# Performance work log

Measured on AMD Instinct MI355X. Metric: run time of the kernel, lower is better.

## Reference

```python
import jax, jax.numpy as jnp
import numpy as np

DIM = 1024
NUM_HEAD = 16
DIM_HEAD = DIM // NUM_HEAD
MAX_SEQ_LEN = 4096
RMS_EPS = 1.1920928955078125e-07  # torch nn.RMSNorm default eps = finfo(fp32).eps
LIN_EPS = 1e-6
PAD_VAL = 1.0
THETA = 10000.0


def rmsnorm(x, g):
    return x * jax.lax.rsqrt(jnp.mean(x * x, axis=-1, keepdims=True) + RMS_EPS) * g


def setup_inputs() -> dict:
    key = jax.random.key(0)
    ks = jax.random.split(key, 20)
    B, L, C, D = 4, 2048, 256, DIM
    s = 1.0 / np.sqrt(D)
    inp = {
        "x": jax.random.normal(ks[0], (B, L, D), jnp.float32),
        "context": jax.random.normal(ks[1], (B, C, D), jnp.float32),
        "attn_mask": jax.random.randint(ks[2], (B, L, L), 0, 2).astype(bool),
        "start_pos": jax.random.randint(ks[3], (B,), 0, MAX_SEQ_LEN - L).astype(jnp.int64),
        "Wqkv": jax.random.normal(ks[4], (D, 3 * D), jnp.float32) * s,
        "bqkv": jax.random.normal(ks[5], (3 * D,), jnp.float32) * 0.01,
        "g_q": jnp.ones((D,), jnp.float32),
        "g_k": jnp.ones((D,), jnp.float32),
        "cWqkv": jax.random.normal(ks[6], (D, 3 * D), jnp.float32) * s,
        "cbqkv": jax.random.normal(ks[7], (3 * D,), jnp.float32) * 0.01,
        "cg_q": jnp.ones((D,), jnp.float32),
        "cg_k": jnp.ones((D,), jnp.float32),
        "Wout": jax.random.normal(ks[8], (D, D), jnp.float32) * s,
        "bout": jax.random.normal(ks[9], (D,), jnp.float32) * 0.01,
        "g_out": jnp.ones((D,), jnp.float32),
        "cWout": jax.random.normal(ks[10], (D, D), jnp.float32) * s,
        "cbout": jax.random.normal(ks[11], (D,), jnp.float32) * 0.01,
        "cg_out": jnp.ones((D,), jnp.float32),
    }
    return inp


def _freqs(pos_indices):
    # pos_indices: (B, L) int
    inv = 1.0 / (THETA ** (jnp.arange(0, DIM_HEAD, 2, dtype=jnp.float32) / DIM_HEAD))  # (DH/2,)
    ang = pos_indices.astype(jnp.float32)[..., None] * inv  # (B, L, DH/2)
    return jnp.cos(ang), jnp.sin(ang)


def _apply_rope(t, cos, sin):
    # t: (B, H, L, DH); cos/sin: (B, L, DH/2) -> broadcast over head
    B, H, L, DH = t.shape
    tr = t.reshape(B, H, L, DH // 2, 2)
    t0, t1 = tr[..., 0], tr[..., 1]
    c = cos[:, None]  # (B,1,L,DH/2)
    s = sin[:, None]
    out = jnp.stack([t0 * c - t1 * s, t0 * s + t1 * c], axis=-1)
    return out.reshape(B, H, L, DH)


def _split_heads(t):
    B, L, D = t.shape
    return t.reshape(B, L, NUM_HEAD, DIM_HEAD).transpose(0, 2, 1, 3)


def _augment_mask(m, C):
    # m: (B, L, L) bool -> (B, L+C, L+C) bool
    B, L, _ = m.shape
    c_to_seq = jnp.broadcast_to(jnp.any(m, axis=1, keepdims=True), (B, C, L))
    seq_to_c = jnp.broadcast_to(jnp.any(m, axis=2, keepdims=True), (B, L, C))
    c_to_c = jnp.ones((B, C, C), bool)
    top = jnp.concatenate([m, seq_to_c], axis=2)
    bot = jnp.concatenate([c_to_seq, c_to_c], axis=2)
    return jnp.concatenate([top, bot], axis=1)


def reference(x, context, attn_mask, start_pos, Wqkv, bqkv, g_q, g_k,
              cWqkv, cbqkv, cg_q, cg_k, Wout, bout, g_out, cWout, cbout, cg_out):
    B, L, D = x.shape
    C = context.shape[1]

    q, k, v = jnp.split(x @ Wqkv + bqkv, 3, axis=-1)
    q = rmsnorm(q, g_q)
    k = rmsnorm(k, g_k)
    q, k, v = _split_heads(q), _split_heads(k), _split_heads(v)  # (B,H,L,DH)

    pos = start_pos[:, None] + jnp.arange(L, dtype=start_pos.dtype)[None]  # (B,L)
    cos, sin = _freqs(pos)
    q = _apply_rope(q, cos, sin)
    k = _apply_rope(k, cos, sin)

    cq, ck, cv = jnp.split(context @ cWqkv + cbqkv, 3, axis=-1)
    cq = rmsnorm(cq, cg_q)
    ck = rmsnorm(ck, cg_k)
    cq, ck, cv = _split_heads(cq), _split_heads(ck), _split_heads(cv)

    q = jnp.concatenate([q, cq], axis=2)  # (B,H,S,DH), S=L+C
    k = jnp.concatenate([k, ck], axis=2)
    v = jnp.concatenate([v, cv], axis=2)

    full_mask = _augment_mask(attn_mask, C)[:, None]  # (B,1,S,S)

    # linear attention: ReLU feature map + padded-value trick
    qf = jax.nn.relu(q)
    kf = jax.nn.relu(k)
    k_mask = full_mask[:, :, 0, :][..., None].astype(kf.dtype)  # (B,1,S,1)
    kf = kf * k_mask
    vpad = jnp.pad(v, ((0, 0), (0, 0), (0, 0), (0, 1)), constant_values=PAD_VAL)  # (B,H,S,DH+1)
    vk = jnp.einsum('bhse,bhsd->bhed', vpad, kf)        # (B,H,DH+1,DH)
    res = jnp.einsum('bhed,bhqd->bhqe', vk, qf)          # (B,H,S,DH+1)
    attn = res[..., :-1] / (res[..., -1:] + LIN_EPS)     # (B,H,S,DH)

    attn = attn.transpose(0, 2, 1, 3).reshape(B, L + C, D)
    x_out = rmsnorm(attn[:, :L] @ Wout + bout, g_out)
    c_out = rmsnorm(attn[:, L:] @ cWout + cbout, cg_out)
    return x_out, c_out
```

## Files before the change

kernel.cpp:

```cpp
#include <hip/hip_runtime.h>

typedef __bf16 bf16;
typedef __bf16 bf16x4 __attribute__((ext_vector_type(4)));
typedef __bf16 bf16x8 __attribute__((ext_vector_type(8)));
typedef float  floatx4 __attribute__((ext_vector_type(4)));

#define L_SEQ   2048
#define C_SEQ   256
#define S_SEQ   2304
#define NBATCH  4
#define NHEAD   16
#define DHEAD   64
#define DMODEL  1024
#define RMS_EPS 1.1920928955078125e-07f
#define LIN_EPS 1e-6f

__device__ __forceinline__ void gload_lds16(const void* g, void* l) {
  __builtin_amdgcn_global_load_lds(
      (const __attribute__((address_space(1))) void*)g,
      (__attribute__((address_space(3))) void*)l, 16, 0, 0);
}

__device__ __forceinline__ void transpose_job(
    const float* __restrict__ src, bf16* __restrict__ dst,
    int R, int C, int tb, bf16 (*tile)[33]) {
  int tilesx = C >> 5;
  int c0 = (tb % tilesx) * 32, r0 = (tb / tilesx) * 32;
  int tx = threadIdx.x & 31, ty = threadIdx.x >> 5;
  for (int i = ty; i < 32; i += 8)
    tile[i][tx] = (bf16)src[(size_t)(r0 + i) * C + c0 + tx];
  __syncthreads();
  for (int i = ty; i < 32; i += 8)
    dst[(size_t)(c0 + i) * R + r0 + tx] = tile[tx][i];
}

__device__ __forceinline__ void convert_job(
    const float* __restrict__ src, bf16* __restrict__ dst, int tb) {
  size_t i = ((size_t)tb * 256 + threadIdx.x) * 8;
  floatx4 a = *(const floatx4*)(src + i);
  floatx4 b = *(const floatx4*)(src + i + 4);
  bf16x8 o;
#pragma unroll
  for (int j = 0; j < 4; j++) { o[j] = (bf16)a[j]; o[4 + j] = (bf16)b[j]; }
  *(bf16x8*)(dst + i) = o;
}

__global__ __launch_bounds__(256) void prep(
    const float* __restrict__ Wqkv, const float* __restrict__ cWqkv,
    const float* __restrict__ Wout, const float* __restrict__ cWout,
    const float* __restrict__ x, const float* __restrict__ ctx,
    const int* __restrict__ mask,
    bf16* __restrict__ WqkvT, bf16* __restrict__ cWqkvT,
    bf16* __restrict__ WoutT, bf16* __restrict__ cWoutT,
    bf16* __restrict__ xbf, bf16* __restrict__ cbf,
    float* __restrict__ vkw, int* __restrict__ anym) {
  __shared__ bf16 tile[32][33];
  __shared__ int sh;
  int b = blockIdx.x;
  if (b < 3072) { transpose_job(Wqkv, WqkvT, 1024, 3072, b, tile); return; }
  b -= 3072;
  if (b < 3072) { transpose_job(cWqkv, cWqkvT, 1024, 3072, b, tile); return; }
  b -= 3072;
  if (b < 1024) { transpose_job(Wout, WoutT, 1024, 1024, b, tile); return; }
  b -= 1024;
  if (b < 1024) { transpose_job(cWout, cWoutT, 1024, 1024, b, tile); return; }
  b -= 1024;
  if (b < 4096) { convert_job(x, xbf, b); return; }
  b -= 4096;
  if (b < 512) { convert_job(ctx, cbf, b); return; }
  b -= 512;
  if (b < 260) {
    int i = b * 1024 + threadIdx.x * 4;
    *(floatx4*)(vkw + i) = floatx4{0.f, 0.f, 0.f, 0.f};
    return;
  }
  b -= 260;
  int a = 0;
  size_t base = (size_t)b * L_SEQ * L_SEQ;
  for (int j = threadIdx.x; j < L_SEQ; j += 256) a |= mask[base + j];
  if (threadIdx.x == 0) sh = 0;
  __syncthreads();
  if (a) atomicOr(&sh, 1);
  __syncthreads();
  if (threadIdx.x == 0) anym[b] = sh;
}

template <bool SCATTER>
__global__ __launch_bounds__(256) void gemm_bias(
    const bf16* __restrict__ A1, const bf16* __restrict__ A2,
    const bf16* __restrict__ B1t, const bf16* __restrict__ B2t,
    const float* __restrict__ bias1, const float* __restrict__ bias2,
    bf16* __restrict__ C1, bf16* __restrict__ C2,
    bf16* __restrict__ qs, bf16* __restrict__ ks, bf16* __restrict__ vs,
    int N, int K, int ybound,
    int rpb1, int soff1, int rpb2, int soff2) {
  __shared__ bf16 As[2][4096];
  __shared__ bf16 Bs[2][4096];

  int nwg = gridDim.x * gridDim.y;
  int wg = blockIdx.y * gridDim.x + blockIdx.x;
  if ((nwg & 7) == 0) {
    int cpx = nwg >> 3;
    wg = (wg & 7) * cpx + (wg >> 3);
  }
  int bx = wg % gridDim.x, by = wg / gridDim.x;
  int n0 = bx * 128;
  const bf16 *Ap, *Bt;
  const float* bias;
  bf16* Cp;
  int m0, rpb, soff;
  if (by < ybound) {
    Ap = A1; Bt = B1t; bias = bias1; Cp = C1;
    m0 = by * 128; rpb = rpb1; soff = soff1;
  } else {
    Ap = A2; Bt = B2t; bias = bias2; Cp = C2;
    m0 = (by - ybound) * 128; rpb = rpb2; soff = soff2;
  }

  int t = threadIdx.x;
  int lane = t & 63, w = t >> 6;
  int wm = (w & 1) * 64, wn = (w >> 1) * 64;
  int l16 = lane & 15, l4 = lane >> 4;

  int srow = w * 32 + (lane >> 2);
  int scol = (lane & 3) * 8;
  const bf16* Ab = Ap + (size_t)(m0 + srow) * K + scol;
  const bf16* Bb = Bt + (size_t)(n0 + srow) * K + scol;

  auto stage = [&](int buf, int kb) {
#pragma unroll
    for (int j = 0; j < 2; j++) {
      gload_lds16(Ab + (size_t)j * 16 * K + kb, (char*)&As[buf][(w * 2 + j) * 512]);
      gload_lds16(Bb + (size_t)j * 16 * K + kb, (char*)&Bs[buf][(w * 2 + j) * 512]);
    }
  };

  floatx4 acc[4][4] = {};
  stage(0, 0);
  __syncthreads();
  int cur = 0;
  for (int kb = 0; kb < K; kb += 32) {
    if (kb + 32 < K) stage(cur ^ 1, kb + 32);
    bf16x8 af[4], bfr[4];
#pragma unroll
    for (int i = 0; i < 4; i++) {
      af[i]  = *(const bf16x8*)&As[cur][(wm + i * 16 + l16) * 32 + l4 * 8];
      bfr[i] = *(const bf16x8*)&Bs[cur][(wn + i * 16 + l16) * 32 + l4 * 8];
    }
#pragma unroll
    for (int i = 0; i < 4; i++)
#pragma unroll
      for (int j = 0; j < 4; j++)
        acc[i][j] = __builtin_amdgcn_mfma_f32_16x16x32_bf16(af[i], bfr[j], acc[i][j], 0, 0, 0);
    __syncthreads();
    cur ^= 1;
  }
#pragma unroll
  for (int i = 0; i < 4; i++)
#pragma unroll
    for (int j = 0; j < 4; j++) {
      int col = n0 + wn + j * 16 + l16;
      float bval = bias[col];
      if constexpr (SCATTER) {
        int which = col >> 10;
        int h = (col >> 6) & 15;
        int dh = col & 63;
        int rmask = (1 << rpb) - 1;
        if (which == 2) {
          int rw0 = m0 + wm + i * 16 + l4 * 4;
          int b = rw0 >> rpb;
          int s = soff + (rw0 & rmask);
          bf16x4 o;
#pragma unroll
          for (int r = 0; r < 4; r++) o[r] = (bf16)(acc[i][j][r] + bval);
          *(bf16x4*)(vs + ((size_t)(b * NHEAD + h) * DHEAD + dh) * S_SEQ + s) = o;
        } else {
          bf16* dst = which == 0 ? qs : ks;
#pragma unroll
          for (int r = 0; r < 4; r++) {
            int rw = m0 + wm + i * 16 + l4 * 4 + r;
            int b = rw >> rpb;
            int s = soff + (rw & rmask);
            dst[((size_t)(b * NHEAD + h) * S_SEQ + s) * DHEAD + dh] =
                (bf16)(acc[i][j][r] + bval);
          }
        }
      } else {
#pragma unroll
        for (int r = 0; r < 4; r++) {
          int rw = m0 + wm + i * 16 + l4 * 4 + r;
          Cp[(size_t)rw * N + col] = (bf16)(acc[i][j][r] + bval);
        }
      }
    }
}

__global__ __launch_bounds__(256) void qkv_post(
    bf16* __restrict__ qs, bf16* __restrict__ ks,
    const int* __restrict__ mask, const int* __restrict__ spos,
    const int* __restrict__ anym,
    const float* __restrict__ g_q, const float* __restrict__ g_k,
    const float* __restrict__ cg_q, const float* __restrict__ cg_k) {
  int g = blockIdx.x, t = threadIdx.x;
  bool is_ctx = g >= NBATCH * L_SEQ;
  int b, s;
  const float *gq, *gk;
  float mval;
  if (!is_ctx) {
    b = g >> 11;
    int l = g & 2047;
    s = l;
    mval = mask[(size_t)b * L_SEQ * L_SEQ + l] ? 1.f : 0.f;
    gq = g_q; gk = g_k;
  } else {
    int gg = g - NBATCH * L_SEQ;
    b = gg >> 8;
    s = L_SEQ + (gg & 255);
    mval = anym[b] ? 1.f : 0.f;
    gq = cg_q; gk = cg_k;
  }
  int d0 = t * 4;
  int h = t >> 4, dh = (t & 15) * 4;
  size_t base = ((size_t)(b * NHEAD + h) * S_SEQ + s) * DHEAD + dh;
  bf16x4 q4 = *(const bf16x4*)(qs + base);
  bf16x4 k4 = *(const bf16x4*)(ks + base);
  float qv[4], kv[4], pq = 0.f, pk = 0.f;
#pragma unroll
  for (int i = 0; i < 4; i++) {
    qv[i] = (float)q4[i]; kv[i] = (float)k4[i];
    pq += qv[i] * qv[i];  pk += kv[i] * kv[i];
  }
  int lane = t & 63, w = t >> 6;
  for (int off = 32; off > 0; off >>= 1) {
    pq += __shfl_down(pq, off, 64);
    pk += __shfl_down(pk, off, 64);
  }
  __shared__ float red[8];
  if (lane == 0) { red[w] = pq; red[4 + w] = pk; }
  __syncthreads();
  float sq = red[0] + red[1] + red[2] + red[3];
  float sk = red[4] + red[5] + red[6] + red[7];
  float scq = rsqrtf(sq * (1.f / DMODEL) + RMS_EPS);
  float sck = rsqrtf(sk * (1.f / DMODEL) + RMS_EPS);
#pragma unroll
  for (int i = 0; i < 4; i++) {
    qv[i] *= scq * gq[d0 + i];
    kv[i] *= sck * gk[d0 + i];
  }
  if (!is_ctx) {
    float p = (float)(spos[b] + s);
#pragma unroll
    for (int pr = 0; pr < 2; pr++) {
      int fi = (dh >> 1) + pr;
      float ang = p * expf((float)fi * -0.28782313662425572f);
      float cc = cosf(ang), ss = sinf(ang);
      float t0 = qv[2 * pr], t1 = qv[2 * pr + 1];
      qv[2 * pr]     = t0 * cc - t1 * ss;
      qv[2 * pr + 1] = t0 * ss + t1 * cc;
      t0 = kv[2 * pr]; t1 = kv[2 * pr + 1];
      kv[2 * pr]     = t0 * cc - t1 * ss;
      kv[2 * pr + 1] = t0 * ss + t1 * cc;
    }
  }
  bf16x4 qo, ko;
#pragma unroll
  for (int i = 0; i < 4; i++) {
    qo[i] = (bf16)fmaxf(qv[i], 0.f);
    ko[i] = (bf16)(fmaxf(kv[i], 0.f) * mval);
  }
  *(bf16x4*)(qs + base) = qo;
  *(bf16x4*)(ks + base) = ko;
}

#define VK_CH   8
#define VK_SPAN (S_SEQ / VK_CH)
__global__ __launch_bounds__(256) void vk_mfma(
    const bf16* __restrict__ vT, const bf16* __restrict__ kf,
    float* __restrict__ vk) {
  __shared__ bf16 Vs[2][64][40];
  __shared__ bf16 Ks[2][64][40];
  int bh = blockIdx.x >> 3, chunk = blockIdx.x & 7;
  int t = threadIdx.x, lane = t & 63, w = t >> 6;
  int l16 = lane & 15, l4 = lane >> 4;
  const bf16* vp = vT + (size_t)bh * DHEAD * S_SEQ;
  const bf16* kp = kf + (size_t)bh * S_SEQ * DHEAD;
  int s_begin = chunk * VK_SPAN;
  int ve = t >> 2, vso = (t & 3) * 8;
  int ks_s = t & 31, kd0 = (t >> 5) * 8;
  floatx4 acc[4] = {};
  float dsum[8] = {};
  bf16x8 vv = *(const bf16x8*)(vp + (size_t)ve * S_SEQ + s_begin + vso);
  bf16x8 kv = *(const bf16x8*)(kp + (size_t)(s_begin + ks_s) * DHEAD + kd0);
  for (int st = 0; st < VK_SPAN; st += 32) {
    int cur = (st >> 5) & 1;
    *(bf16x8*)&Vs[cur][ve][vso] = vv;
#pragma unroll
    for (int j = 0; j < 8; j++) {
      Ks[cur][kd0 + j][ks_s] = kv[j];
      dsum[j] += (float)kv[j];
    }
    if (st + 32 < VK_SPAN) {
      int s0 = s_begin + st + 32;
      vv = *(const bf16x8*)(vp + (size_t)ve * S_SEQ + s0 + vso);
      kv = *(const bf16x8*)(kp + (size_t)(s0 + ks_s) * DHEAD + kd0);
    }
    __syncthreads();
    bf16x8 af = *(const bf16x8*)&Vs[cur][w * 16 + l16][l4 * 8];
#pragma unroll
    for (int nt = 0; nt < 4; nt++) {
      bf16x8 bfr = *(const bf16x8*)&Ks[cur][nt * 16 + l16][l4 * 8];
      acc[nt] = __builtin_amdgcn_mfma_f32_16x16x32_bf16(af, bfr, acc[nt], 0, 0, 0);
    }
  }
  float* vkbh = vk + (size_t)bh * 65 * 64;
#pragma unroll
  for (int nt = 0; nt < 4; nt++)
#pragma unroll
    for (int r = 0; r < 4; r++)
      atomicAdd(&vkbh[(w * 16 + l4 * 4 + r) * 64 + nt * 16 + l16], acc[nt][r]);
#pragma unroll
  for (int j = 0; j < 8; j++)
#pragma unroll
    for (int off = 16; off > 0; off >>= 1)
      dsum[j] += __shfl_down(dsum[j], off, 32);
  if ((lane & 31) == 0)
#pragma unroll
    for (int j = 0; j < 8; j++)
      atomicAdd(&vkbh[64 * 64 + kd0 + j], dsum[j]);
}

__global__ __launch_bounds__(256) void res_attn(
    const bf16* __restrict__ qf, const float* __restrict__ vk,
    bf16* __restrict__ attn_x, bf16* __restrict__ attn_c) {
  __shared__ bf16 Bs[80][72];
  __shared__ float sden[256];
  int bh = blockIdx.x / 9, mblk = blockIdx.x % 9;
  int b = bh >> 4, h = bh & 15;
  int t = threadIdx.x, lane = t & 63, w = t >> 6;
  const float* vkp = vk + (size_t)bh * 65 * 64;
  for (int i = t; i < 80 * 64; i += 256) {
    int e = i >> 6, d = i & 63;
    Bs[e][d] = (bf16)(e < 65 ? vkp[i] : 0.f);
  }
  __syncthreads();
  int l16 = lane & 15, l4 = lane >> 4;
  const bf16* qbase = qf + (size_t)bh * S_SEQ * DHEAD;
  int q0w = mblk * 256 + w * 64;

  floatx4 acc[4][5] = {};
  bf16x8 af[4][2], bfr[5][2];
#pragma unroll
  for (int mt = 0; mt < 4; mt++) {
    int q = q0w + mt * 16 + l16;
    af[mt][0] = *(const bf16x8*)(qbase + (size_t)q * 64 + l4 * 8);
    af[mt][1] = *(const bf16x8*)(qbase + (size_t)q * 64 + 32 + l4 * 8);
  }
#pragma unroll
  for (int nt = 0; nt < 5; nt++) {
    bfr[nt][0] = *(const bf16x8*)&Bs[nt * 16 + l16][l4 * 8];
    bfr[nt][1] = *(const bf16x8*)&Bs[nt * 16 + l16][32 + l4 * 8];
  }
#pragma unroll
  for (int mt = 0; mt < 4; mt++)
#pragma unroll
    for (int nt = 0; nt < 5; nt++) {
      acc[mt][nt] = __builtin_amdgcn_mfma_f32_16x16x32_bf16(af[mt][0], bfr[nt][0], acc[mt][nt], 0, 0, 0);
      acc[mt][nt] = __builtin_amdgcn_mfma_f32_16x16x32_bf16(af[mt][1], bfr[nt][1], acc[mt][nt], 0, 0, 0);
    }
  if (l16 == 0) {
#pragma unroll
    for (int mt = 0; mt < 4; mt++)
#pragma unroll
      for (int r = 0; r < 4; r++)
        sden[w * 64 + mt * 16 + l4 * 4 + r] = acc[mt][4][r];
  }
  __syncthreads();
#pragma unroll
  for (int mt = 0; mt < 4; mt++)
#pragma unroll
    for (int r = 0; r < 4; r++) {
      float den = sden[w * 64 + mt * 16 + l4 * 4 + r] + LIN_EPS;
      float rden = 1.f / den;
      int q = q0w + mt * 16 + l4 * 4 + r;
#pragma unroll
      for (int nt = 0; nt < 4; nt++) {
        int dcol = nt * 16 + l16;
        float a = acc[mt][nt][r] * rden;
        if (q < L_SEQ)
          attn_x[((size_t)b * L_SEQ + q) * DMODEL + h * DHEAD + dcol] = (bf16)a;
        else
          attn_c[((size_t)b * C_SEQ + (q - L_SEQ)) * DMODEL + h * DHEAD + dcol] = (bf16)a;
      }
    }
}

__global__ __launch_bounds__(256) void final_norm(
    const bf16* __restrict__ y_x, const bf16* __restrict__ y_c,
    const float* __restrict__ g_out, const float* __restrict__ cg_out,
    float* __restrict__ out) {
  int g = blockIdx.x, t = threadIdx.x;
  const bf16* src;
  const float* gv;
  if (g < NBATCH * L_SEQ) {
    src = y_x + (size_t)g * DMODEL; gv = g_out;
  } else {
    int gg = g - NBATCH * L_SEQ;
    src = y_c + (size_t)gg * DMODEL; gv = cg_out;
  }
  float* dst = out + (size_t)g * DMODEL;
  int d0 = t * 4;
  bf16x4 y4 = *(const bf16x4*)(src + d0);
  float yv[4], p = 0.f;
#pragma unroll
  for (int i = 0; i < 4; i++) { yv[i] = (float)y4[i]; p += yv[i] * yv[i]; }
  int lane = t & 63, w = t >> 6;
  for (int off = 32; off > 0; off >>= 1) p += __shfl_down(p, off, 64);
  __shared__ float red[4];
  if (lane == 0) red[w] = p;
  __syncthreads();
  float ssum = red[0] + red[1] + red[2] + red[3];
  float sc = rsqrtf(ssum * (1.f / DMODEL) + RMS_EPS);
  floatx4 o;
#pragma unroll
  for (int i = 0; i < 4; i++) o[i] = yv[i] * sc * gv[d0 + i];
  *(floatx4*)(dst + d0) = o;
}

extern "C" void kernel_launch(void* const* d_in, const int* in_sizes, int n_in,
                              void* d_out, int out_size, void* d_ws, size_t ws_size,
                              hipStream_t stream) {
  const float* x      = (const float*)d_in[0];
  const float* ctx    = (const float*)d_in[1];
  const int*   mask   = (const int*)d_in[2];
  const int*   spos   = (const int*)d_in[3];
  const float* Wqkv   = (const float*)d_in[4];
  const float* bqkv   = (const float*)d_in[5];
  const float* g_q    = (const float*)d_in[6];
  const float* g_k    = (const float*)d_in[7];
  const float* cWqkv  = (const float*)d_in[8];
  const float* cbqkv  = (const float*)d_in[9];
  const float* cg_q   = (const float*)d_in[10];
  const float* cg_k   = (const float*)d_in[11];
  const float* Wout   = (const float*)d_in[12];
  const float* bout   = (const float*)d_in[13];
  const float* g_out  = (const float*)d_in[14];
  const float* cWout  = (const float*)d_in[15];
  const float* cbout  = (const float*)d_in[16];
  const float* cg_out = (const float*)d_in[17];

  char* wsp = (char*)d_ws;
  size_t off = 0;
  auto alloc = [&](size_t bytes) -> void* {
    void* p = wsp + off;
    off += (bytes + 255) & ~(size_t)255;
    return p;
  };
  bf16* WqkvT  = (bf16*)alloc((size_t)3072 * 1024 * 2);
  bf16* cWqkvT = (bf16*)alloc((size_t)3072 * 1024 * 2);
  bf16* WoutT  = (bf16*)alloc((size_t)1024 * 1024 * 2);
  bf16* cWoutT = (bf16*)alloc((size_t)1024 * 1024 * 2);
  bf16* xbf    = (bf16*)alloc((size_t)NBATCH * L_SEQ * DMODEL * 2);
  bf16* cbf    = (bf16*)alloc((size_t)NBATCH * C_SEQ * DMODEL * 2);
  const size_t SLAB = (size_t)NBATCH * NHEAD * S_SEQ * DHEAD;
  bf16* qfs    = (bf16*)alloc(SLAB * 2);
  bf16* kfs    = (bf16*)alloc(SLAB * 2);
  bf16* vfs    = (bf16*)alloc(SLAB * 2);
  float* vkw   = (float*)alloc((size_t)64 * 65 * 64 * 4);
  int* anym    = (int*)alloc(256);
  bf16* attn_x = kfs;
  bf16* attn_c = kfs + (size_t)NBATCH * L_SEQ * DMODEL;
  bf16* y_x    = vfs;
  bf16* y_c    = vfs + (size_t)NBATCH * L_SEQ * DMODEL;

  prep<<<13064, 256, 0, stream>>>(Wqkv, cWqkv, Wout, cWout, x, ctx, mask,
                                  WqkvT, cWqkvT, WoutT, cWoutT, xbf, cbf,
                                  vkw, anym);

  gemm_bias<true><<<dim3(24, 72), 256, 0, stream>>>(
      xbf, cbf, WqkvT, cWqkvT, bqkv, cbqkv, nullptr, nullptr,
      qfs, kfs, vfs, 3072, 1024, 64, 11, 0, 8, L_SEQ);

  qkv_post<<<NBATCH * (L_SEQ + C_SEQ), 256, 0, stream>>>(
      qfs, kfs, mask, spos, anym, g_q, g_k, cg_q, cg_k);

  vk_mfma<<<64 * VK_CH, 256, 0, stream>>>(vfs, kfs, vkw);

  res_attn<<<576, 256, 0, stream>>>(qfs, vkw, attn_x, attn_c);

  gemm_bias<false><<<dim3(8, 72), 256, 0, stream>>>(
      attn_x, attn_c, WoutT, cWoutT, bout, cbout, y_x, y_c,
      nullptr, nullptr, nullptr, 1024, 1024, 64, 0, 0, 0, 0);

  final_norm<<<NBATCH * (L_SEQ + C_SEQ), 256, 0, stream>>>(
      y_x, y_c, g_out, cg_out, (float*)d_out);
}
```

Measured before the change: 356.6 us.

## Enlarge GEMM tiles to 256x256 with swizzled LDS and precompute RoPE table

The GEMM kernel moves from 128x128 tiles with 4 waves and a K-step of 32 to 256x256 tiles with 8 waves and a K-step of 64. It adds an XOR-swizzled LDS layout to avoid bank conflicts and raises wave priority around the MFMA block. This aims to cut global/LDS traffic per FLOP, but each block now uses 128 KB of LDS, which limits occupancy, and the grids become much smaller (432 and 144 blocks), which may under-fill the GPU. Separately, RoPE cos/sin values are computed once in the prep kernel and stored in a table, so qkv_post reads them instead of calling expf, sinf and cosf per element.

New measurement: 350.3 us. No clear change (-1.8%).

```diff
diff --git a/kernel.cpp b/kernel.cpp
--- a/kernel.cpp
+++ b/kernel.cpp
@@ -49,11 +49,12 @@
     const float* __restrict__ Wqkv, const float* __restrict__ cWqkv,
     const float* __restrict__ Wout, const float* __restrict__ cWout,
     const float* __restrict__ x, const float* __restrict__ ctx,
-    const int* __restrict__ mask,
+    const int* __restrict__ mask, const int* __restrict__ spos,
     bf16* __restrict__ WqkvT, bf16* __restrict__ cWqkvT,
     bf16* __restrict__ WoutT, bf16* __restrict__ cWoutT,
     bf16* __restrict__ xbf, bf16* __restrict__ cbf,
-    float* __restrict__ vkw, int* __restrict__ anym) {
+    float* __restrict__ vkw, float* __restrict__ rope,
+    int* __restrict__ anym) {
   __shared__ bf16 tile[32][33];
   __shared__ int sh;
   int b = blockIdx.x;
@@ -75,6 +76,16 @@
     return;
   }
   b -= 260;
+  if (b < 2048) {
+    int t = threadIdx.x;
+    int tok = b * 4 + (t >> 6);
+    int bb = tok >> 11, s = tok & 2047;
+    int j = t & 63, fi = j >> 1;
+    float ang = (float)(spos[bb] + s) * expf((float)fi * -0.28782313662425572f);
+    rope[(size_t)tok * 64 + j] = (j & 1) ? sinf(ang) : cosf(ang);
+    return;
+  }
+  b -= 2048;
   int a = 0;
   size_t base = (size_t)b * L_SEQ * L_SEQ;
   for (int j = threadIdx.x; j < L_SEQ; j += 256) a |= mask[base + j];
@@ -86,7 +97,7 @@
 }
 
 template <bool SCATTER>
-__global__ __launch_bounds__(256) void gemm_bias(
+__global__ __launch_bounds__(512, 2) void gemm_bias(
     const bf16* __restrict__ A1, const bf16* __restrict__ A2,
     const bf16* __restrict__ B1t, const bf16* __restrict__ B2t,
     const float* __restrict__ bias1, const float* __restrict__ bias2,
@@ -94,72 +105,91 @@
     bf16* __restrict__ qs, bf16* __restrict__ ks, bf16* __restrict__ vs,
     int N, int K, int ybound,
     int rpb1, int soff1, int rpb2, int soff2) {
-  __shared__ bf16 As[2][4096];
-  __shared__ bf16 Bs[2][4096];
+  __shared__ bf16 As[2][16384];
+  __shared__ bf16 Bs[2][16384];
 
   int nwg = gridDim.x * gridDim.y;
   int wg = blockIdx.y * gridDim.x + blockIdx.x;
-  if ((nwg & 7) == 0) {
-    int cpx = nwg >> 3;
-    wg = (wg & 7) * cpx + (wg >> 3);
-  }
+  int cpx = nwg >> 3;
+  wg = (wg & 7) * cpx + (wg >> 3);
   int bx = wg % gridDim.x, by = wg / gridDim.x;
-  int n0 = bx * 128;
+  int n0 = bx * 256;
   const bf16 *Ap, *Bt;
   const float* bias;
   bf16* Cp;
   int m0, rpb, soff;
   if (by < ybound) {
     Ap = A1; Bt = B1t; bias = bias1; Cp = C1;
-    m0 = by * 128; rpb = rpb1; soff = soff1;
+    m0 = by * 256; rpb = rpb1; soff = soff1;
   } else {
     Ap = A2; Bt = B2t; bias = bias2; Cp = C2;
-    m0 = (by - ybound) * 128; rpb = rpb2; soff = soff2;
-  }
-
-  int t = threadIdx.x;
-  int lane = t & 63, w = t >> 6;
-  int wm = (w & 1) * 64, wn = (w >> 1) * 64;
+    m0 = (by - ybound) * 256; rpb = rpb2; soff = soff2;
+  }
+
+  int t = threadIdx.x, lane = t & 63, w = t >> 6;
+  int wr = w >> 2, wc = w & 3;
   int l16 = lane & 15, l4 = lane >> 4;
 
-  int srow = w * 32 + (lane >> 2);
-  int scol = (lane & 3) * 8;
+  int srow = w * 32 + (lane >> 3);
+  int scol = ((lane & 7) ^ (lane >> 3)) << 3;
   const bf16* Ab = Ap + (size_t)(m0 + srow) * K + scol;
   const bf16* Bb = Bt + (size_t)(n0 + srow) * K + scol;
 
-  auto stage = [&](int buf, int kb) {
-#pragma unroll
-    for (int j = 0; j < 2; j++) {
-      gload_lds16(Ab + (size_t)j * 16 * K + kb, (char*)&As[buf][(w * 2 + j) * 512]);
-      gload_lds16(Bb + (size_t)j * 16 * K + kb, (char*)&Bs[buf][(w * 2 + j) * 512]);
-    }
-  };
-
-  floatx4 acc[4][4] = {};
-  stage(0, 0);
-  __syncthreads();
-  int cur = 0;
-  for (int kb = 0; kb < K; kb += 32) {
-    if (kb + 32 < K) stage(cur ^ 1, kb + 32);
-    bf16x8 af[4], bfr[4];
-#pragma unroll
-    for (int i = 0; i < 4; i++) {
-      af[i]  = *(const bf16x8*)&As[cur][(wm + i * 16 + l16) * 32 + l4 * 8];
-      bfr[i] = *(const bf16x8*)&Bs[cur][(wn + i * 16 + l16) * 32 + l4 * 8];
-    }
-#pragma unroll
-    for (int i = 0; i < 4; i++)
-#pragma unroll
-      for (int j = 0; j < 4; j++)
-        acc[i][j] = __builtin_amdgcn_mfma_f32_16x16x32_bf16(af[i], bfr[j], acc[i][j], 0, 0, 0);
+  int co0 = (l4 * 8) ^ ((l16 & 7) << 3);
+  int co1 = (32 + l4 * 8) ^ ((l16 & 7) << 3);
+  int rba = (wr * 128 + l16) * 64;
+  int rbb = (wc * 64 + l16) * 64;
+
+  floatx4 acc[8][4] = {};
+
+#pragma unroll
+  for (int j = 0; j < 4; j++) {
+    gload_lds16(Ab + (size_t)j * 8 * K, (char*)As + w * 4096 + j * 1024);
+    gload_lds16(Bb + (size_t)j * 8 * K, (char*)Bs + w * 4096 + j * 1024);
+  }
+  __syncthreads();
+
+  int NT = K >> 6;
+  for (int tt = 0; tt < NT; ++tt) {
+    int p = tt & 1;
+    if (tt + 1 < NT) {
+      int kb = (tt + 1) << 6;
+#pragma unroll
+      for (int j = 0; j < 4; j++) {
+        gload_lds16(Ab + (size_t)j * 8 * K + kb,
+                    (char*)As + (p ^ 1) * 32768 + w * 4096 + j * 1024);
+        gload_lds16(Bb + (size_t)j * 8 * K + kb,
+                    (char*)Bs + (p ^ 1) * 32768 + w * 4096 + j * 1024);
+      }
+    }
+    const bf16* Asp = As[p];
+    const bf16* Bsp = Bs[p];
+    bf16x8 b0[4], b1[4];
+#pragma unroll
+    for (int nt = 0; nt < 4; nt++) {
+      b0[nt] = *(const bf16x8*)&Bsp[rbb + nt * 1024 + co0];
+      b1[nt] = *(const bf16x8*)&Bsp[rbb + nt * 1024 + co1];
+    }
+    __builtin_amdgcn_s_setprio(1);
+#pragma unroll
+    for (int mt = 0; mt < 8; mt++) {
+      bf16x8 a0 = *(const bf16x8*)&Asp[rba + mt * 1024 + co0];
+      bf16x8 a1 = *(const bf16x8*)&Asp[rba + mt * 1024 + co1];
+#pragma unroll
+      for (int nt = 0; nt < 4; nt++) {
+        acc[mt][nt] = __builtin_amdgcn_mfma_f32_16x16x32_bf16(a0, b0[nt], acc[mt][nt], 0, 0, 0);
+        acc[mt][nt] = __builtin_amdgcn_mfma_f32_16x16x32_bf16(a1, b1[nt], acc[mt][nt], 0, 0, 0);
+      }
+    }
+    __builtin_amdgcn_s_setprio(0);
     __syncthreads();
-    cur ^= 1;
-  }
-#pragma unroll
-  for (int i = 0; i < 4; i++)
-#pragma unroll
-    for (int j = 0; j < 4; j++) {
-      int col = n0 + wn + j * 16 + l16;
+  }
+
+#pragma unroll
+  for (int mt = 0; mt < 8; mt++)
+#pragma unroll
+    for (int nt = 0; nt < 4; nt++) {
+      int col = n0 + wc * 64 + nt * 16 + l16;
       float bval = bias[col];
       if constexpr (SCATTER) {
         int which = col >> 10;
@@ -167,29 +197,29 @@
         int dh = col & 63;
         int rmask = (1 << rpb) - 1;
         if (which == 2) {
-          int rw0 = m0 + wm + i * 16 + l4 * 4;
+          int rw0 = m0 + wr * 128 + mt * 16 + l4 * 4;
           int b = rw0 >> rpb;
           int s = soff + (rw0 & rmask);
           bf16x4 o;
 #pragma unroll
-          for (int r = 0; r < 4; r++) o[r] = (bf16)(acc[i][j][r] + bval);
+          for (int r = 0; r < 4; r++) o[r] = (bf16)(acc[mt][nt][r] + bval);
           *(bf16x4*)(vs + ((size_t)(b * NHEAD + h) * DHEAD + dh) * S_SEQ + s) = o;
         } else {
           bf16* dst = which == 0 ? qs : ks;
 #pragma unroll
           for (int r = 0; r < 4; r++) {
-            int rw = m0 + wm + i * 16 + l4 * 4 + r;
+            int rw = m0 + wr * 128 + mt * 16 + l4 * 4 + r;
             int b = rw >> rpb;
             int s = soff + (rw & rmask);
             dst[((size_t)(b * NHEAD + h) * S_SEQ + s) * DHEAD + dh] =
-                (bf16)(acc[i][j][r] + bval);
+                (bf16)(acc[mt][nt][r] + bval);
           }
         }
       } else {
 #pragma unroll
         for (int r = 0; r < 4; r++) {
-          int rw = m0 + wm + i * 16 + l4 * 4 + r;
-          Cp[(size_t)rw * N + col] = (bf16)(acc[i][j][r] + bval);
+          int rw = m0 + wr * 128 + mt * 16 + l4 * 4 + r;
+          Cp[(size_t)rw * N + col] = (bf16)(acc[mt][nt][r] + bval);
         }
       }
     }
@@ -197,7 +227,7 @@
 
 __global__ __launch_bounds__(256) void qkv_post(
     bf16* __restrict__ qs, bf16* __restrict__ ks,
-    const int* __restrict__ mask, const int* __restrict__ spos,
+    const int* __restrict__ mask, const float* __restrict__ rope,
     const int* __restrict__ anym,
     const float* __restrict__ g_q, const float* __restrict__ g_k,
     const float* __restrict__ cg_q, const float* __restrict__ cg_k) {
@@ -248,12 +278,10 @@
     kv[i] *= sck * gk[d0 + i];
   }
   if (!is_ctx) {
-    float p = (float)(spos[b] + s);
+    floatx4 tb4 = *(const floatx4*)&rope[((size_t)(b << 11 | s)) * 64 + dh];
 #pragma unroll
     for (int pr = 0; pr < 2; pr++) {
-      int fi = (dh >> 1) + pr;
-      float ang = p * expf((float)fi * -0.28782313662425572f);
-      float cc = cosf(ang), ss = sinf(ang);
+      float cc = tb4[2 * pr], ss = tb4[2 * pr + 1];
       float t0 = qv[2 * pr], t1 = qv[2 * pr + 1];
       qv[2 * pr]     = t0 * cc - t1 * ss;
       qv[2 * pr + 1] = t0 * ss + t1 * cc;
@@ -466,30 +494,31 @@
   bf16* kfs    = (bf16*)alloc(SLAB * 2);
   bf16* vfs    = (bf16*)alloc(SLAB * 2);
   float* vkw   = (float*)alloc((size_t)64 * 65 * 64 * 4);
+  float* rope  = (float*)alloc((size_t)NBATCH * L_SEQ * 64 * 4);
   int* anym    = (int*)alloc(256);
   bf16* attn_x = kfs;
   bf16* attn_c = kfs + (size_t)NBATCH * L_SEQ * DMODEL;
   bf16* y_x    = vfs;
   bf16* y_c    = vfs + (size_t)NBATCH * L_SEQ * DMODEL;
 
-  prep<<<13064, 256, 0, stream>>>(Wqkv, cWqkv, Wout, cWout, x, ctx, mask,
+  prep<<<15112, 256, 0, stream>>>(Wqkv, cWqkv, Wout, cWout, x, ctx, mask, spos,
                                   WqkvT, cWqkvT, WoutT, cWoutT, xbf, cbf,
-                                  vkw, anym);
-
-  gemm_bias<true><<<dim3(24, 72), 256, 0, stream>>>(
+                                  vkw, rope, anym);
+
+  gemm_bias<true><<<dim3(12, 36), 512, 0, stream>>>(
       xbf, cbf, WqkvT, cWqkvT, bqkv, cbqkv, nullptr, nullptr,
-      qfs, kfs, vfs, 3072, 1024, 64, 11, 0, 8, L_SEQ);
+      qfs, kfs, vfs, 3072, 1024, 32, 11, 0, 8, L_SEQ);
 
   qkv_post<<<NBATCH * (L_SEQ + C_SEQ), 256, 0, stream>>>(
-      qfs, kfs, mask, spos, anym, g_q, g_k, cg_q, cg_k);
+      qfs, kfs, mask, rope, anym, g_q, g_k, cg_q, cg_k);
 
   vk_mfma<<<64 * VK_CH, 256, 0, stream>>>(vfs, kfs, vkw);
 
   res_attn<<<576, 256, 0, stream>>>(qfs, vkw, attn_x, attn_c);
 
-  gemm_bias<false><<<dim3(8, 72), 256, 0, stream>>>(
+  gemm_bias<false><<<dim3(4, 36), 512, 0, stream>>>(
       attn_x, attn_c, WoutT, cWoutT, bout, cbout, y_x, y_c,
-      nullptr, nullptr, nullptr, 1024, 1024, 64, 0, 0, 0, 0);
+      nullptr, nullptr, nullptr, 1024, 1024, 32, 0, 0, 0, 0);
 
   final_norm<<<NBATCH * (L_SEQ + C_SEQ), 256, 0, stream>>>(
       y_x, y_c, g_out, cg_out, (float*)d_out);
```
